# Kernel optimization log

Hardware: AMD Instinct MI355X
Metric: run time of the kernel (lower is better)

Reference implementation:

```python
import jax, jax.numpy as jnp
import numpy as np

B, M, N, DIM, P, Q, OUT = 64, 64, 64, 3, 3, 3, 512


def gen_knot_vector(p, n):
    # p leading zeros + linspace(0,1,n-p) + p trailing ones (repo convention)
    return np.concatenate([np.zeros(p), np.linspace(0.0, 1.0, n - p), np.ones(p)])


def precompute_basis(n_ctrl, p, out_dim):
    """Knot spans and Cox-de Boor basis values (Piegl A2.1/A2.2) on a uniform param grid."""
    U = gen_knot_vector(p, n_ctrl)
    u = np.linspace(0.0, 1.0, out_dim)
    # largest i with U[i] <= u, clamped to the valid span range [p, n_ctrl-2]
    spans = np.clip(np.searchsorted(U, u, side='right') - 1, p, n_ctrl - 2)
    Nmat = np.zeros((out_dim, p + 1))
    for i in range(out_dim):
        s, uu = int(spans[i]), u[i]
        Ni = np.zeros(p + 1); Ni[0] = 1.0
        left = np.zeros(p + 1); right = np.zeros(p + 1)
        for j in range(1, p + 1):
            left[j] = uu - U[s + 1 - j]
            right[j] = U[s + j] - uu
            saved = 0.0
            for r in range(j):
                temp = Ni[r] / (right[r + 1] + left[j - r])
                Ni[r] = saved + right[r + 1] * temp
                saved = left[j - r] * temp
            Ni[j] = saved
        Nmat[i] = Ni
    # gather index table: control-point row span-p+l for l in 0..p
    idx = spans[:, None] - p + np.arange(p + 1)[None, :]
    return Nmat.astype(np.float32), idx.astype(np.int64)


def setup_inputs() -> dict:
    key = jax.random.key(0)
    k1, k2 = jax.random.split(key)
    xyz = jax.random.normal(k1, (B, M, N, DIM), dtype=jnp.float32)
    w = jax.random.uniform(k2, (B, M, N, 1), dtype=jnp.float32, minval=0.5, maxval=1.5)
    ctrl = jnp.concatenate([xyz, w], axis=-1)  # homogeneous control points [B,M,N,4]
    Nu, iu = precompute_basis(M, P, OUT)
    Nv, iv = precompute_basis(N, Q, OUT)
    return {"ctrl": ctrl, "Nu": jnp.asarray(Nu), "Nv": jnp.asarray(Nv),
            "iu": jnp.asarray(iu), "iv": jnp.asarray(iv)}


def reference(ctrl, Nu, Nv, iu, iv):
    D = ctrl.shape[-1] - 1
    U_, V_ = Nu.shape[0], Nv.shape[0]
    surf = jnp.zeros((ctrl.shape[0], U_, V_, ctrl.shape[-1]), dtype=ctrl.dtype)
    for l in range(iu.shape[1]):          # p+1 terms (fixed, small)
        rows = ctrl[:, iu[:, l]]          # [B, U, N, D+1]
        for r in range(iv.shape[1]):      # q+1 terms (fixed, small)
            pts = rows[:, :, iv[:, r]]    # [B, U, V, D+1]
            w = Nu[:, l][:, None] * Nv[None, :, r]  # [U, V]
            surf = surf + w[None, :, :, None] * pts
    return surf[..., :D] / surf[..., D:]  # perspective divide
```

## Files before the change

kernel.cpp:

```cpp
#include <hip/hip_runtime.h>


#define OUTDIM 512
#define CTRL_N 64
#define TU 8

__global__ __launch_bounds__(256) void surf_eval_kernel(
    const float* __restrict__ ctrl,
    const float* __restrict__ Nu,
    const float* __restrict__ Nv,
    const int*   __restrict__ iu,
    const int*   __restrict__ iv,
    float*       __restrict__ out)
{
    __shared__ float4 rows[TU * CTRL_N];

    const int blk = blockIdx.x;
    const int b  = blk >> 6;
    const int U0 = (blk & 63) * TU;
    const int t  = threadIdx.x;

    {
        const int u  = t >> 5;
        const int n0 = t & 31;
        const int U  = U0 + u;
        const float4 nu  = *(const float4*)(Nu + U * 4);
        const int4   iu4 = *(const int4*)(iu + U * 4);
        const float* cb = ctrl + (size_t)b * (64 * 64 * 4);
        const float* r0 = cb + (size_t)iu4.x * (CTRL_N * 4);
        const float* r1 = cb + (size_t)iu4.y * (CTRL_N * 4);
        const float* r2 = cb + (size_t)iu4.z * (CTRL_N * 4);
        const float* r3 = cb + (size_t)iu4.w * (CTRL_N * 4);

#pragma unroll
        for (int k = 0; k < 2; ++k) {
            const int n = n0 + 32 * k;
            const float4 p0 = *(const float4*)(r0 + n * 4);
            const float4 p1 = *(const float4*)(r1 + n * 4);
            const float4 p2 = *(const float4*)(r2 + n * 4);
            const float4 p3 = *(const float4*)(r3 + n * 4);
            float4 acc;
            acc.x = nu.x * p0.x + nu.y * p1.x + nu.z * p2.x + nu.w * p3.x;
            acc.y = nu.x * p0.y + nu.y * p1.y + nu.z * p2.y + nu.w * p3.y;
            acc.z = nu.x * p0.z + nu.y * p1.z + nu.z * p2.z + nu.w * p3.z;
            acc.w = nu.x * p0.w + nu.y * p1.w + nu.z * p2.w + nu.w * p3.w;
            rows[u * CTRL_N + n] = acc;
        }
    }
    __syncthreads();

    const float4 nvA = *(const float4*)(Nv + t * 4);
    const int4   ivA = *(const int4*)(iv + t * 4);
    const float4 nvB = *(const float4*)(Nv + (t + 256) * 4);
    const int4   ivB = *(const int4*)(iv + (t + 256) * 4);

    const size_t obase = ((size_t)b * OUTDIM + U0) * OUTDIM;

#pragma unroll
    for (int u = 0; u < TU; ++u) {
        const float4* ru = rows + u * CTRL_N;

        {
            const float4 q0 = ru[ivA.x];
            const float4 q1 = ru[ivA.y];
            const float4 q2 = ru[ivA.z];
            const float4 q3 = ru[ivA.w];
            float sx = nvA.x * q0.x + nvA.y * q1.x + nvA.z * q2.x + nvA.w * q3.x;
            float sy = nvA.x * q0.y + nvA.y * q1.y + nvA.z * q2.y + nvA.w * q3.y;
            float sz = nvA.x * q0.z + nvA.y * q1.z + nvA.z * q2.z + nvA.w * q3.z;
            float sw = nvA.x * q0.w + nvA.y * q1.w + nvA.z * q2.w + nvA.w * q3.w;
            const float inv = __builtin_amdgcn_rcpf(sw);
            const size_t o = (obase + (size_t)u * OUTDIM + t) * 3;
            out[o + 0] = sx * inv;
            out[o + 1] = sy * inv;
            out[o + 2] = sz * inv;
        }
        {
            const float4 q0 = ru[ivB.x];
            const float4 q1 = ru[ivB.y];
            const float4 q2 = ru[ivB.z];
            const float4 q3 = ru[ivB.w];
            float sx = nvB.x * q0.x + nvB.y * q1.x + nvB.z * q2.x + nvB.w * q3.x;
            float sy = nvB.x * q0.y + nvB.y * q1.y + nvB.z * q2.y + nvB.w * q3.y;
            float sz = nvB.x * q0.z + nvB.y * q1.z + nvB.z * q2.z + nvB.w * q3.z;
            float sw = nvB.x * q0.w + nvB.y * q1.w + nvB.z * q2.w + nvB.w * q3.w;
            const float inv = __builtin_amdgcn_rcpf(sw);
            const size_t o = (obase + (size_t)u * OUTDIM + t + 256) * 3;
            out[o + 0] = sx * inv;
            out[o + 1] = sy * inv;
            out[o + 2] = sz * inv;
        }
    }
}

extern "C" void kernel_launch(void* const* d_in, const int* in_sizes, int n_in,
                              void* d_out, int out_size, void* d_ws, size_t ws_size,
                              hipStream_t stream) {
    const float* ctrl = (const float*)d_in[0];
    const float* Nu   = (const float*)d_in[1];
    const float* Nv   = (const float*)d_in[2];
    const int*   iu   = (const int*)d_in[3];
    const int*   iv   = (const int*)d_in[4];
    float* out = (float*)d_out;

    const int nblocks = 64 * (OUTDIM / TU);
    surf_eval_kernel<<<nblocks, 256, 0, stream>>>(ctrl, Nu, Nv, iu, iv, out);
}
```

Measured before the change: 204.4 us.

## Compute 4 consecutive outputs per thread with shared span window and float4 stores

```diff
diff --git a/kernel.cpp b/kernel.cpp
--- a/kernel.cpp
+++ b/kernel.cpp
@@ -49,47 +49,54 @@
     }
     __syncthreads();
 
-    const float4 nvA = *(const float4*)(Nv + t * 4);
-    const int4   ivA = *(const int4*)(iv + t * 4);
-    const float4 nvB = *(const float4*)(Nv + (t + 256) * 4);
-    const int4   ivB = *(const int4*)(iv + (t + 256) * 4);
+    const int q  = t & 127;
+    const int V0 = q * 4;
+    const int u0 = (t >> 7) * 4;
+
+    float4 nv[4];
+    int    d[4];
+    const int s0 = iv[(size_t)V0 * 4];
+#pragma unroll
+    for (int j = 0; j < 4; ++j) {
+        nv[j] = *(const float4*)(Nv + (V0 + j) * 4);
+        d[j]  = iv[(size_t)(V0 + j) * 4] - s0;
+    }
 
     const size_t obase = ((size_t)b * OUTDIM + U0) * OUTDIM;
 
 #pragma unroll
-    for (int u = 0; u < TU; ++u) {
-        const float4* ru = rows + u * CTRL_N;
+    for (int uu = 0; uu < 4; ++uu) {
+        const int u = u0 + uu;
+        const float4* ru = rows + u * CTRL_N + s0;
 
-        {
-            const float4 q0 = ru[ivA.x];
-            const float4 q1 = ru[ivA.y];
-            const float4 q2 = ru[ivA.z];
-            const float4 q3 = ru[ivA.w];
-            float sx = nvA.x * q0.x + nvA.y * q1.x + nvA.z * q2.x + nvA.w * q3.x;
-            float sy = nvA.x * q0.y + nvA.y * q1.y + nvA.z * q2.y + nvA.w * q3.y;
-            float sz = nvA.x * q0.z + nvA.y * q1.z + nvA.z * q2.z + nvA.w * q3.z;
-            float sw = nvA.x * q0.w + nvA.y * q1.w + nvA.z * q2.w + nvA.w * q3.w;
+        float4 qb0 = ru[0], qb1 = ru[1], qb2 = ru[2], qb3 = ru[3], qb4 = ru[4];
+
+        float px[4], py[4], pz[4];
+#pragma unroll
+        for (int j = 0; j < 4; ++j) {
+            const bool sh = (d[j] != 0);
+            const float4 w0 = sh ? qb1 : qb0;
+            const float4 w1 = sh ? qb2 : qb1;
+            const float4 w2 = sh ? qb3 : qb2;
+            const float4 w3 = sh ? qb4 : qb3;
+            const float4 n4 = nv[j];
+            float sx = n4.x * w0.x + n4.y * w1.x + n4.z * w2.x + n4.w * w3.x;
+            float sy = n4.x * w0.y + n4.y * w1.y + n4.z * w2.y + n4.w * w3.y;
+            float sz = n4.x * w0.z + n4.y * w1.z + n4.z * w2.z + n4.w * w3.z;
+            float sw = n4.x * w0.w + n4.y * w1.w + n4.z * w2.w + n4.w * w3.w;
             const float inv = __builtin_amdgcn_rcpf(sw);
-            const size_t o = (obase + (size_t)u * OUTDIM + t) * 3;
-            out[o + 0] = sx * inv;
-            out[o + 1] = sy * inv;
-            out[o + 2] = sz * inv;
+            px[j] = sx * inv;
+            py[j] = sy * inv;
+            pz[j] = sz * inv;
         }
-        {
-            const float4 q0 = ru[ivB.x];
-            const float4 q1 = ru[ivB.y];
-            const float4 q2 = ru[ivB.z];
-            const float4 q3 = ru[ivB.w];
-            float sx = nvB.x * q0.x + nvB.y * q1.x + nvB.z * q2.x + nvB.w * q3.x;
-            float sy = nvB.x * q0.y + nvB.y * q1.y + nvB.z * q2.y + nvB.w * q3.y;
-            float sz = nvB.x * q0.z + nvB.y * q1.z + nvB.z * q2.z + nvB.w * q3.z;
-            float sw = nvB.x * q0.w + nvB.y * q1.w + nvB.z * q2.w + nvB.w * q3.w;
-            const float inv = __builtin_amdgcn_rcpf(sw);
-            const size_t o = (obase + (size_t)u * OUTDIM + t + 256) * 3;
-            out[o + 0] = sx * inv;
-            out[o + 1] = sy * inv;
-            out[o + 2] = sz * inv;
-        }
+
+        float* o = out + (obase + (size_t)u * OUTDIM + V0) * 3;
+        float4 s0v = {px[0], py[0], pz[0], px[1]};
+        float4 s1v = {py[1], pz[1], px[2], py[2]};
+        float4 s2v = {pz[2], px[3], py[3], pz[3]};
+        ((float4*)o)[0] = s0v;
+        ((float4*)o)[1] = s1v;
+        ((float4*)o)[2] = s2v;
     }
 }
 
```

Result: slower. 228.3 us (+11.7%).
